# Kernel tuning notes

Hardware: AMD Instinct MI355X
Metric: run time of the kernel (lower is better)

## Reference

```python
import jax, jax.numpy as jnp
import numpy as np

CH = 256            # channels
IN_C = CH // 2      # 128
INTER_C = CH // 16  # 16
NUM_POINTS = 32
BN_EPS = 1e-5


def conv1x1(x, W, b=None):
    # x: [B,C,H,W], W: [O,C]
    y = jnp.einsum('oc,bchw->bohw', W, x)
    if b is not None:
        y = y + b[None, :, None, None]
    return y


def bilinear_sample(feat, sx, sy):
    """feat [B,C,H,W]; sx,sy [B,N,P] continuous index coords; border padding."""
    B, C, H, W = feat.shape
    x0f = jnp.floor(sx)
    y0f = jnp.floor(sy)
    wx = sx - x0f
    wy = sy - y0f
    x0 = jnp.clip(x0f.astype(jnp.int32), 0, W - 1)
    x1 = jnp.clip(x0f.astype(jnp.int32) + 1, 0, W - 1)
    y0 = jnp.clip(y0f.astype(jnp.int32), 0, H - 1)
    y1 = jnp.clip(y0f.astype(jnp.int32) + 1, 0, H - 1)
    feat_f = feat.reshape(B, C, H * W).transpose(0, 2, 1)  # [B,HW,C]

    def gather(yi, xi):
        idx = (yi * W + xi).reshape(B, -1)  # [B,N*P]
        return jnp.take_along_axis(feat_f, idx[:, :, None], axis=1)  # [B,N*P,C]

    wxf = wx.reshape(B, -1, 1)
    wyf = wy.reshape(B, -1, 1)
    out = (gather(y0, x0) * (1 - wxf) * (1 - wyf)
           + gather(y0, x1) * wxf * (1 - wyf)
           + gather(y1, x0) * (1 - wxf) * wyf
           + gather(y1, x1) * wxf * wyf)
    N, P = sx.shape[1], sx.shape[2]
    return out.reshape(B, N, P, C)


def multi_scale_attention(qf, vf, Wq, bq, Wk, bk, Wv, bv, Woff, boff):
    # deformable-style point-sampling attention with NUM_POINTS samples per query
    B, _, H, W = qf.shape
    N = H * W
    q = conv1x1(qf, Wq, bq).reshape(B, INTER_C, N).transpose(0, 2, 1)  # [B,N,Ci]
    k = conv1x1(vf, Wk, bk)                                            # [B,Ci,H,W]
    v = conv1x1(vf, Wv, bv)                                            # [B,Cv,H,W]
    off = conv1x1(qf, Woff, boff).reshape(B, NUM_POINTS, 2, N)
    off = off.transpose(0, 3, 1, 2)                                    # [B,N,P,2] (dx,dy)
    ys, xs = jnp.meshgrid(jnp.arange(H, dtype=qf.dtype),
                          jnp.arange(W, dtype=qf.dtype), indexing='ij')
    sx = xs.reshape(-1)[None, :, None] + off[..., 0]                   # [B,N,P]
    sy = ys.reshape(-1)[None, :, None] + off[..., 1]
    k_s = bilinear_sample(k, sx, sy)                                   # [B,N,P,Ci]
    v_s = bilinear_sample(v, sx, sy)                                   # [B,N,P,Cv]
    logits = jnp.einsum('bnc,bnpc->bnp', q, k_s) / jnp.sqrt(jnp.asarray(INTER_C, qf.dtype))
    attn = jax.nn.softmax(logits, axis=-1)
    out = jnp.einsum('bnp,bnpc->bnc', attn, v_s)                       # [B,N,Cv]
    return out.transpose(0, 2, 1).reshape(B, -1, H, W)


def setup_inputs() -> dict:
    key = jax.random.key(0)
    ks = jax.random.split(key, 12)
    B, Hl, Wl, Hh, Wh = 2, 64, 64, 32, 32
    s = 0.02
    return {
        'low_feature': jax.random.normal(ks[0], (B, CH, Hl, Wl), jnp.float32),
        'high_feature': jax.random.normal(ks[1], (B, CH, Hh, Wh), jnp.float32),
        'W1': jax.random.normal(ks[2], (IN_C, 2 * CH), jnp.float32) * s,
        'b1': jnp.zeros((IN_C,), jnp.float32),
        'W2': jax.random.normal(ks[3], (IN_C, CH), jnp.float32) * s,
        'b2': jnp.zeros((IN_C,), jnp.float32),
        'Wq': jax.random.normal(ks[4], (INTER_C, IN_C), jnp.float32) * s,
        'bq': jnp.zeros((INTER_C,), jnp.float32),
        'Wk': jax.random.normal(ks[5], (INTER_C, IN_C), jnp.float32) * s,
        'bk': jnp.zeros((INTER_C,), jnp.float32),
        'Wv': jax.random.normal(ks[6], (IN_C, IN_C), jnp.float32) * s,
        'bv': jnp.zeros((IN_C,), jnp.float32),
        'Woff': jax.random.normal(ks[7], (2 * NUM_POINTS, IN_C), jnp.float32) * 0.5,
        'boff': jnp.zeros((2 * NUM_POINTS,), jnp.float32),
        'Wb': jax.random.normal(ks[8], (CH, IN_C + CH), jnp.float32) * s,
        'gamma': jnp.ones((CH,), jnp.float32),
        'beta': jnp.zeros((CH,), jnp.float32),
        'rmean': jnp.zeros((CH,), jnp.float32),
        'rvar': jnp.ones((CH,), jnp.float32),
    }


def reference(low_feature, high_feature, W1, b1, W2, b2, Wq, bq, Wk, bk,
              Wv, bv, Woff, boff, Wb, gamma, beta, rmean, rvar):
    B, _, Hl, Wl = low_feature.shape
    # F.interpolate(mode='bilinear', align_corners=False) == jax.image half-pixel bilinear
    high_up = jax.image.resize(high_feature, (B, CH, Hl, Wl), method='bilinear')
    query_feature = conv1x1(jnp.concatenate([high_up, low_feature], axis=1), W1, b1)
    value_feature = conv1x1(high_up, W2, b2)
    value_feature = multi_scale_attention(query_feature, value_feature,
                                          Wq, bq, Wk, bk, Wv, bv, Woff, boff)
    x = conv1x1(jnp.concatenate([value_feature, high_up], axis=1), Wb)
    # BatchNorm (eval form) + ReLU
    x = (x - rmean[None, :, None, None]) * jax.lax.rsqrt(rvar + BN_EPS)[None, :, None, None]
    x = x * gamma[None, :, None, None] + beta[None, :, None, None]
    return jax.nn.relu(x)
```

## Files before the change

kernel.cpp:

```cpp
#include <hip/hip_runtime.h>
#include <hip/hip_bf16.h>

#define NL 4096
#define HH 32
#define WH 32

typedef __attribute__((ext_vector_type(8))) short s8v;
typedef __attribute__((ext_vector_type(4))) short s4v;
typedef __attribute__((ext_vector_type(4))) float f32x4;

static __device__ inline unsigned short f2bf(float x) {
  __hip_bfloat16 h = __float2bfloat16(x);
  return *reinterpret_cast<unsigned short*>(&h);
}
static __device__ inline float bfbits2f(unsigned int lo16) {
  unsigned int u = lo16 << 16;
  return *reinterpret_cast<float*>(&u);
}

__global__ __launch_bounds__(256) void convert_weights_k(
    const float* __restrict__ w1, const float* __restrict__ w2,
    const float* __restrict__ wq, const float* __restrict__ woff,
    const float* __restrict__ wk, const float* __restrict__ wv,
    const float* __restrict__ wb, short* __restrict__ dst) {
  int i = blockIdx.x * 256 + threadIdx.x;
  const float* src; int off;
  if      (i <  65536) { src = w1;   off = 0; }
  else if (i <  98304) { src = w2;   off = 65536; }
  else if (i < 100352) { src = wq;   off = 98304; }
  else if (i < 108544) { src = woff; off = 100352; }
  else if (i < 110592) { src = wk;   off = 108544; }
  else if (i < 126976) { src = wv;   off = 110592; }
  else if (i < 225280) { src = wb;   off = 126976; }
  else return;
  dst[i] = (short)f2bf(src[i - off]);
}

__global__ __launch_bounds__(256) void k1_fused(
    const float* __restrict__ low, const float* __restrict__ high,
    const short* __restrict__ wc,
    const float* __restrict__ b1, const float* __restrict__ b2,
    const float* __restrict__ bq, const float* __restrict__ boff,
    const float* __restrict__ bk, const float* __restrict__ bv,
    short* __restrict__ xh, float* __restrict__ q_t, float* __restrict__ k_t,
    float* __restrict__ off_t, short* __restrict__ v_t) {
  __shared__ short xin_s[16 * 520];
  __shared__ short qf_s[16 * 136];
  __shared__ short vf_s[16 * 136];
  const int tid = threadIdx.x;
  const int pix0 = blockIdx.x * 16;
  const int b = pix0 >> 12;
  const int n0 = pix0 & (NL - 1);

  {
    const int nl = tid & 15, cg = tid >> 4;
    const int n = n0 + nl;
    const int y = n >> 6, x = n & 63;
    float sx = x * 0.5f - 0.25f;
    float sy = y * 0.5f - 0.25f;
    float x0f = floorf(sx), y0f = floorf(sy);
    float wx = sx - x0f, wy = sy - y0f;
    int x0i = (int)x0f, y0i = (int)y0f;
    int x0c = min(WH - 1, max(0, x0i)), x1c = min(WH - 1, max(0, x0i + 1));
    int y0c = min(HH - 1, max(0, y0i)), y1c = min(HH - 1, max(0, y0i + 1));
    float w00 = (1.f - wy) * (1.f - wx), w01 = (1.f - wy) * wx;
    float w10 = wy * (1.f - wx),         w11 = wy * wx;
#pragma unroll
    for (int i = 0; i < 16; i++) {
      int c = cg * 16 + i;
      const float* f = high + (size_t)(b * 256 + c) * (HH * WH);
      float v = w00 * f[y0c * WH + x0c] + w01 * f[y0c * WH + x1c]
              + w10 * f[y1c * WH + x0c] + w11 * f[y1c * WH + x1c];
      xin_s[nl * 520 + c] = (short)f2bf(v);
      xin_s[nl * 520 + 256 + c] =
          (short)f2bf(low[(size_t)(b * 256 + c) * NL + n]);
    }
  }
  __syncthreads();

  {
    const int r = tid >> 4, c0 = (tid & 15) * 16;
    s8v v0 = *(const s8v*)(xin_s + r * 520 + c0);
    s8v v1 = *(const s8v*)(xin_s + r * 520 + c0 + 8);
    *(s8v*)(xh + (size_t)(pix0 + r) * 256 + c0) = v0;
    *(s8v*)(xh + (size_t)(pix0 + r) * 256 + c0 + 8) = v1;
  }

  const int wave = tid >> 6, lane = tid & 63;
  const int quad = lane >> 4, id = lane & 15;

  {
    f32x4 acc0 = (f32x4){0.f, 0.f, 0.f, 0.f};
    f32x4 acc1 = (f32x4){0.f, 0.f, 0.f, 0.f};
    const short* a0 = wc + (size_t)(wave * 32 + id) * 512 + quad * 8;
    const short* a1 = a0 + 16 * 512;
    const short* bp = xin_s + id * 520 + quad * 8;
#pragma unroll
    for (int kk = 0; kk < 512; kk += 32) {
      s8v bf = *(const s8v*)(bp + kk);
      acc0 = __builtin_amdgcn_mfma_f32_16x16x32_bf16(*(const s8v*)(a0 + kk), bf, acc0, 0, 0, 0);
      acc1 = __builtin_amdgcn_mfma_f32_16x16x32_bf16(*(const s8v*)(a1 + kk), bf, acc1, 0, 0, 0);
    }
    int m0 = wave * 32 + quad * 4;
    s4v o0, o1;
#pragma unroll
    for (int r = 0; r < 4; r++) {
      o0[r] = (short)f2bf(acc0[r] + b1[m0 + r]);
      o1[r] = (short)f2bf(acc1[r] + b1[m0 + 16 + r]);
    }
    *(s4v*)(qf_s + id * 136 + m0) = o0;
    *(s4v*)(qf_s + id * 136 + m0 + 16) = o1;
  }

  {
    f32x4 acc0 = (f32x4){0.f, 0.f, 0.f, 0.f};
    f32x4 acc1 = (f32x4){0.f, 0.f, 0.f, 0.f};
    const short* a0 = wc + 65536 + (size_t)(wave * 32 + id) * 256 + quad * 8;
    const short* a1 = a0 + 16 * 256;
    const short* bp = xin_s + id * 520 + quad * 8;
#pragma unroll
    for (int kk = 0; kk < 256; kk += 32) {
      s8v bf = *(const s8v*)(bp + kk);
      acc0 = __builtin_amdgcn_mfma_f32_16x16x32_bf16(*(const s8v*)(a0 + kk), bf, acc0, 0, 0, 0);
      acc1 = __builtin_amdgcn_mfma_f32_16x16x32_bf16(*(const s8v*)(a1 + kk), bf, acc1, 0, 0, 0);
    }
    int m0 = wave * 32 + quad * 4;
    s4v o0, o1;
#pragma unroll
    for (int r = 0; r < 4; r++) {
      o0[r] = (short)f2bf(acc0[r] + b2[m0 + r]);
      o1[r] = (short)f2bf(acc1[r] + b2[m0 + 16 + r]);
    }
    *(s4v*)(vf_s + id * 136 + m0) = o0;
    *(s4v*)(vf_s + id * 136 + m0 + 16) = o1;
  }
  __syncthreads();

  for (int f = wave; f < 14; f += 4) {
    const short* ap = wc + 98304 + (size_t)(f * 16 + id) * 128 + quad * 8;
    const short* bp = (f < 5 ? qf_s : vf_s) + id * 136 + quad * 8;
    f32x4 acc = (f32x4){0.f, 0.f, 0.f, 0.f};
#pragma unroll
    for (int kk = 0; kk < 128; kk += 32)
      acc = __builtin_amdgcn_mfma_f32_16x16x32_bf16(
          *(const s8v*)(ap + kk), *(const s8v*)(bp + kk), acc, 0, 0, 0);
    const int pix = pix0 + id;
    const int mq = quad * 4;
    if (f == 0) {
      f32x4 v;
#pragma unroll
      for (int r = 0; r < 4; r++) v[r] = acc[r] + bq[mq + r];
      *(f32x4*)(q_t + (size_t)pix * 16 + mq) = v;
    } else if (f < 5) {
      int m = (f - 1) * 16 + mq;
      f32x4 v;
#pragma unroll
      for (int r = 0; r < 4; r++) v[r] = acc[r] + boff[m + r];
      *(f32x4*)(off_t + (size_t)pix * 64 + m) = v;
    } else if (f == 5) {
      f32x4 v;
#pragma unroll
      for (int r = 0; r < 4; r++) v[r] = acc[r] + bk[mq + r];
      *(f32x4*)(k_t + (size_t)pix * 16 + mq) = v;
    } else {
      int m = (f - 6) * 16 + mq;
      s4v o;
#pragma unroll
      for (int r = 0; r < 4; r++) o[r] = (short)f2bf(acc[r] + bv[m + r]);
      *(s4v*)(v_t + (size_t)pix * 128 + m) = o;
    }
  }
}

__global__ __launch_bounds__(256) void k2_fused(
    const float* __restrict__ q_t, const float* __restrict__ k_t,
    const short* __restrict__ v_t, const float* __restrict__ off_t,
    const short* __restrict__ xh, const short* __restrict__ wb,
    const float* __restrict__ gamma, const float* __restrict__ beta,
    const float* __restrict__ rmean, const float* __restrict__ rvar,
    float* __restrict__ out) {
  __shared__ float s_w[4][32][4];
  __shared__ int   s_i[4][32][4];
  __shared__ short attn_s[16 * 136];
  const int tid = threadIdx.x;
  const int wave = tid >> 6, lane = tid & 63;
  const int pix0 = blockIdx.x * 16;

  const int pt = lane >> 1, h = lane & 1;
  const int c = 2 * lane;
  for (int jj = 0; jj < 4; jj++) {
    const int qidx = pix0 + wave * 4 + jj;
    const int b = qidx >> 12;
    const int n = qidx & (NL - 1);
    const int qy = n >> 6, qx = n & 63;

    const float* qp = q_t + (size_t)qidx * 16;
    float qreg[16];
#pragma unroll
    for (int i = 0; i < 16; i += 4) {
      float4 t = *(const float4*)(qp + i);
      qreg[i] = t.x; qreg[i + 1] = t.y; qreg[i + 2] = t.z; qreg[i + 3] = t.w;
    }

    float2 dxy = *(const float2*)(off_t + (size_t)qidx * 64 + 2 * pt);
    float sx = (float)qx + dxy.x;
    float sy = (float)qy + dxy.y;
    float x0f = floorf(sx), y0f = floorf(sy);
    float wx = sx - x0f, wy = sy - y0f;
    int x0i = (int)x0f, y0i = (int)y0f;
    int x0 = min(63, max(0, x0i)), x1 = min(63, max(0, x0i + 1));
    int y0 = min(63, max(0, y0i)), y1 = min(63, max(0, y0i + 1));

    int   yr  = h ? y1 : y0;
    float wyr = h ? wy : (1.f - wy);
    int   pa = yr * 64 + x0, pb = yr * 64 + x1;
    float wa = wyr * (1.f - wx), wb_ = wyr * wx;

    const float* kb = k_t + (size_t)b * NL * 16;
    float da = 0.f, db = 0.f;
    {
      const float* ka = kb + (size_t)pa * 16;
      const float* kc = kb + (size_t)pb * 16;
#pragma unroll
      for (int i = 0; i < 16; i += 4) {
        float4 a4 = *(const float4*)(ka + i);
        float4 c4 = *(const float4*)(kc + i);
        da = fmaf(qreg[i], a4.x, da); da = fmaf(qreg[i + 1], a4.y, da);
        da = fmaf(qreg[i + 2], a4.z, da); da = fmaf(qreg[i + 3], a4.w, da);
        db = fmaf(qreg[i], c4.x, db); db = fmaf(qreg[i + 1], c4.y, db);
        db = fmaf(qreg[i + 2], c4.z, db); db = fmaf(qreg[i + 3], c4.w, db);
      }
    }
    float part = wa * da + wb_ * db;
    part += __shfl_xor(part, 1, 64);
    float logit = part * 0.25f;

    float m = logit;
#pragma unroll
    for (int s = 32; s > 0; s >>= 1) m = fmaxf(m, __shfl_xor(m, s, 64));
    float e = __expf(logit - m);
    float ssum = e;
#pragma unroll
    for (int s = 32; s > 0; s >>= 1) ssum += __shfl_xor(ssum, s, 64);
    float a = e * 2.f / ssum;

    s_w[wave][pt][2 * h + 0] = a * wa;
    s_w[wave][pt][2 * h + 1] = a * wb_;
    s_i[wave][pt][2 * h + 0] = pa;
    s_i[wave][pt][2 * h + 1] = pb;

    const short* vb = v_t + (size_t)b * NL * 128;
    float o0 = 0.f, o1 = 0.f;
    for (int pp = 0; pp < 32; pp++) {
#pragma unroll
      for (int t = 0; t < 4; t++) {
        float w  = s_w[wave][pp][t];
        int  pix = s_i[wave][pp][t];
        unsigned int u = *(const unsigned int*)(vb + (size_t)pix * 128 + c);
        o0 = fmaf(w, bfbits2f(u & 0xffffu), o0);
        o1 = fmaf(w, bfbits2f(u >> 16), o1);
      }
    }
    unsigned int pk = (unsigned int)f2bf(o0) | ((unsigned int)f2bf(o1) << 16);
    *(unsigned int*)(attn_s + (wave * 4 + jj) * 136 + c) = pk;
  }
  __syncthreads();

  const int quad = lane >> 4, id = lane & 15;
  const int m0 = wave * 64;
  const int pix = pix0 + id;

  s8v bfr[12];
#pragma unroll
  for (int k4 = 0; k4 < 4; k4++)
    bfr[k4] = *(const s8v*)(attn_s + id * 136 + quad * 8 + k4 * 32);
#pragma unroll
  for (int k8 = 0; k8 < 8; k8++)
    bfr[4 + k8] = *(const s8v*)(xh + (size_t)pix * 256 + quad * 8 + k8 * 32);

  f32x4 acc[4];
#pragma unroll
  for (int mf = 0; mf < 4; mf++) acc[mf] = (f32x4){0.f, 0.f, 0.f, 0.f};
  const short* ap[4];
#pragma unroll
  for (int mf = 0; mf < 4; mf++)
    ap[mf] = wb + (size_t)(m0 + mf * 16 + id) * 384 + quad * 8;

#pragma unroll
  for (int k = 0; k < 12; k++) {
#pragma unroll
    for (int mf = 0; mf < 4; mf++)
      acc[mf] = __builtin_amdgcn_mfma_f32_16x16x32_bf16(
          *(const s8v*)(ap[mf] + k * 32), bfr[k], acc[mf], 0, 0, 0);
  }

  const int bb = pix >> 12, nlow = pix & (NL - 1);
#pragma unroll
  for (int mf = 0; mf < 4; mf++) {
    int mbase = m0 + mf * 16 + quad * 4;
#pragma unroll
    for (int r = 0; r < 4; r++) {
      int o = mbase + r;
      float s  = gamma[o] * rsqrtf(rvar[o] + 1e-5f);
      float sh = beta[o] - rmean[o] * s;
      out[((size_t)bb * 256 + o) * NL + nlow] = fmaxf(fmaf(acc[mf][r], s, sh), 0.f);
    }
  }
}

extern "C" void kernel_launch(void* const* d_in, const int* in_sizes, int n_in,
                              void* d_out, int out_size, void* d_ws, size_t ws_size,
                              hipStream_t stream) {
  const float* low   = (const float*)d_in[0];
  const float* high  = (const float*)d_in[1];
  const float* W1    = (const float*)d_in[2];
  const float* b1    = (const float*)d_in[3];
  const float* W2    = (const float*)d_in[4];
  const float* b2    = (const float*)d_in[5];
  const float* Wq    = (const float*)d_in[6];
  const float* bq    = (const float*)d_in[7];
  const float* Wk    = (const float*)d_in[8];
  const float* bk    = (const float*)d_in[9];
  const float* Wv    = (const float*)d_in[10];
  const float* bv    = (const float*)d_in[11];
  const float* Woff  = (const float*)d_in[12];
  const float* boff  = (const float*)d_in[13];
  const float* Wb    = (const float*)d_in[14];
  const float* gamma = (const float*)d_in[15];
  const float* beta  = (const float*)d_in[16];
  const float* rmean = (const float*)d_in[17];
  const float* rvar  = (const float*)d_in[18];
  float* out = (float*)d_out;

  short* ws    = (short*)d_ws;
  short* xh    = ws;
  short* v_t   = xh + 2097152;
  short* wc    = v_t + 1048576;
  float* q_t   = (float*)(wc + 225280);
  float* k_t   = q_t + 131072;
  float* off_t = k_t + 131072;

  convert_weights_k<<<880, 256, 0, stream>>>(W1, W2, Wq, Woff, Wk, Wv, Wb, wc);
  k1_fused<<<512, 256, 0, stream>>>(low, high, wc, b1, b2, bq, boff, bk, bv,
                                    xh, q_t, k_t, off_t, v_t);
  k2_fused<<<512, 256, 0, stream>>>(q_t, k_t, v_t, off_t, xh, wc + 126976,
                                    gamma, beta, rmean, rvar, out);
}
```

Before: 160.4 us.

## Use 1024-thread blocks with one query per wave and 16-byte value gathers

k2_fused now launches 16 waves per block, so each wave handles a single query pixel instead of looping over four. The value aggregation has each lane load 8 bf16 channels (uint4) for one of the four bilinear corners, then sums across corners with cross-lane shuffles. The output GEMM gives each wave one 16-row M tile instead of four. The aim is more parallelism and wider gathers to hide gather latency, at the cost of extra shuffle reductions, a larger block that syncs 16 waves at once, and register pressure from the fully unrolled loop.

```diff
diff --git a/kernel.cpp b/kernel.cpp
--- a/kernel.cpp
+++ b/kernel.cpp
@@ -172,24 +172,22 @@
   }
 }
 
-__global__ __launch_bounds__(256) void k2_fused(
+__global__ __launch_bounds__(1024, 2) void k2_fused(
     const float* __restrict__ q_t, const float* __restrict__ k_t,
     const short* __restrict__ v_t, const float* __restrict__ off_t,
     const short* __restrict__ xh, const short* __restrict__ wb,
     const float* __restrict__ gamma, const float* __restrict__ beta,
     const float* __restrict__ rmean, const float* __restrict__ rvar,
     float* __restrict__ out) {
-  __shared__ float s_w[4][32][4];
-  __shared__ int   s_i[4][32][4];
+  __shared__ float s_w[16][32][4];
+  __shared__ int   s_i[16][32][4];
   __shared__ short attn_s[16 * 136];
   const int tid = threadIdx.x;
   const int wave = tid >> 6, lane = tid & 63;
   const int pix0 = blockIdx.x * 16;
 
-  const int pt = lane >> 1, h = lane & 1;
-  const int c = 2 * lane;
-  for (int jj = 0; jj < 4; jj++) {
-    const int qidx = pix0 + wave * 4 + jj;
+  {
+    const int qidx = pix0 + wave;
     const int b = qidx >> 12;
     const int n = qidx & (NL - 1);
     const int qy = n >> 6, qx = n & 63;
@@ -202,6 +200,7 @@
       qreg[i] = t.x; qreg[i + 1] = t.y; qreg[i + 2] = t.z; qreg[i + 3] = t.w;
     }
 
+    const int pt = lane >> 1, h = lane & 1;
     float2 dxy = *(const float2*)(off_t + (size_t)qidx * 64 + 2 * pt);
     float sx = (float)qx + dxy.x;
     float sy = (float)qy + dxy.y;
@@ -249,61 +248,67 @@
     s_i[wave][pt][2 * h + 0] = pa;
     s_i[wave][pt][2 * h + 1] = pb;
 
-    const short* vb = v_t + (size_t)b * NL * 128;
-    float o0 = 0.f, o1 = 0.f;
+    const int t = lane >> 4, chunk = lane & 15;
+    const short* vb = v_t + (size_t)b * NL * 128 + chunk * 8;
+    float o[8];
+#pragma unroll
+    for (int j = 0; j < 8; j++) o[j] = 0.f;
+#pragma unroll
     for (int pp = 0; pp < 32; pp++) {
-#pragma unroll
-      for (int t = 0; t < 4; t++) {
-        float w  = s_w[wave][pp][t];
-        int  pix = s_i[wave][pp][t];
-        unsigned int u = *(const unsigned int*)(vb + (size_t)pix * 128 + c);
-        o0 = fmaf(w, bfbits2f(u & 0xffffu), o0);
-        o1 = fmaf(w, bfbits2f(u >> 16), o1);
-      }
-    }
-    unsigned int pk = (unsigned int)f2bf(o0) | ((unsigned int)f2bf(o1) << 16);
-    *(unsigned int*)(attn_s + (wave * 4 + jj) * 136 + c) = pk;
+      float w_ = s_w[wave][pp][t];
+      int  pix = s_i[wave][pp][t];
+      uint4 u = *(const uint4*)(vb + (size_t)pix * 128);
+      o[0] = fmaf(w_, bfbits2f(u.x & 0xffffu), o[0]);
+      o[1] = fmaf(w_, bfbits2f(u.x >> 16),     o[1]);
+      o[2] = fmaf(w_, bfbits2f(u.y & 0xffffu), o[2]);
+      o[3] = fmaf(w_, bfbits2f(u.y >> 16),     o[3]);
+      o[4] = fmaf(w_, bfbits2f(u.z & 0xffffu), o[4]);
+      o[5] = fmaf(w_, bfbits2f(u.z >> 16),     o[5]);
+      o[6] = fmaf(w_, bfbits2f(u.w & 0xffffu), o[6]);
+      o[7] = fmaf(w_, bfbits2f(u.w >> 16),     o[7]);
+    }
+#pragma unroll
+    for (int j = 0; j < 8; j++) {
+      o[j] += __shfl_xor(o[j], 16, 64);
+      o[j] += __shfl_xor(o[j], 32, 64);
+    }
+    if (t == 0) {
+      uint4 pk;
+      pk.x = (unsigned)f2bf(o[0]) | ((unsigned)f2bf(o[1]) << 16);
+      pk.y = (unsigned)f2bf(o[2]) | ((unsigned)f2bf(o[3]) << 16);
+      pk.z = (unsigned)f2bf(o[4]) | ((unsigned)f2bf(o[5]) << 16);
+      pk.w = (unsigned)f2bf(o[6]) | ((unsigned)f2bf(o[7]) << 16);
+      *(uint4*)(attn_s + wave * 136 + chunk * 8) = pk;
+    }
   }
   __syncthreads();
 
-  const int quad = lane >> 4, id = lane & 15;
-  const int m0 = wave * 64;
-  const int pix = pix0 + id;
-
-  s8v bfr[12];
-#pragma unroll
-  for (int k4 = 0; k4 < 4; k4++)
-    bfr[k4] = *(const s8v*)(attn_s + id * 136 + quad * 8 + k4 * 32);
-#pragma unroll
-  for (int k8 = 0; k8 < 8; k8++)
-    bfr[4 + k8] = *(const s8v*)(xh + (size_t)pix * 256 + quad * 8 + k8 * 32);
-
-  f32x4 acc[4];
-#pragma unroll
-  for (int mf = 0; mf < 4; mf++) acc[mf] = (f32x4){0.f, 0.f, 0.f, 0.f};
-  const short* ap[4];
-#pragma unroll
-  for (int mf = 0; mf < 4; mf++)
-    ap[mf] = wb + (size_t)(m0 + mf * 16 + id) * 384 + quad * 8;
-
-#pragma unroll
-  for (int k = 0; k < 12; k++) {
-#pragma unroll
-    for (int mf = 0; mf < 4; mf++)
-      acc[mf] = __builtin_amdgcn_mfma_f32_16x16x32_bf16(
-          *(const s8v*)(ap[mf] + k * 32), bfr[k], acc[mf], 0, 0, 0);
-  }
-
-  const int bb = pix >> 12, nlow = pix & (NL - 1);
-#pragma unroll
-  for (int mf = 0; mf < 4; mf++) {
-    int mbase = m0 + mf * 16 + quad * 4;
+  {
+    const int quad = lane >> 4, id = lane & 15;
+    const int m0 = wave * 16;
+    const int pix = pix0 + id;
+
+    f32x4 acc = (f32x4){0.f, 0.f, 0.f, 0.f};
+    const short* ap = wb + (size_t)(m0 + id) * 384 + quad * 8;
+    const short* bs = attn_s + id * 136 + quad * 8;
+    const short* bg = xh + (size_t)pix * 256 + quad * 8;
+#pragma unroll
+    for (int k = 0; k < 4; k++)
+      acc = __builtin_amdgcn_mfma_f32_16x16x32_bf16(
+          *(const s8v*)(ap + k * 32), *(const s8v*)(bs + k * 32), acc, 0, 0, 0);
+#pragma unroll
+    for (int k = 0; k < 8; k++)
+      acc = __builtin_amdgcn_mfma_f32_16x16x32_bf16(
+          *(const s8v*)(ap + 128 + k * 32), *(const s8v*)(bg + k * 32), acc, 0, 0, 0);
+
+    const int bb = pix >> 12, nlow = pix & (NL - 1);
+    const int mbase = m0 + quad * 4;
 #pragma unroll
     for (int r = 0; r < 4; r++) {
       int o = mbase + r;
       float s  = gamma[o] * rsqrtf(rvar[o] + 1e-5f);
       float sh = beta[o] - rmean[o] * s;
-      out[((size_t)bb * 256 + o) * NL + nlow] = fmaxf(fmaf(acc[mf][r], s, sh), 0.f);
+      out[((size_t)bb * 256 + o) * NL + nlow] = fmaxf(fmaf(acc[r], s, sh), 0.f);
     }
   }
 }
@@ -343,6 +348,6 @@
   convert_weights_k<<<880, 256, 0, stream>>>(W1, W2, Wq, Woff, Wk, Wv, Wb, wc);
   k1_fused<<<512, 256, 0, stream>>>(low, high, wc, b1, b2, bq, boff, bk, bv,
                                     xh, q_t, k_t, off_t, v_t);
-  k2_fused<<<512, 256, 0, stream>>>(q_t, k_t, v_t, off_t, xh, wc + 126976,
-                                    gamma, beta, rmean, rvar, out);
-}
+  k2_fused<<<512, 1024, 0, stream>>>(q_t, k_t, v_t, off_t, xh, wc + 126976,
+                                     gamma, beta, rmean, rvar, out);
+}
```

Measured after the change: 155.4 us, median of 2. -3.1%, faster.
